# Performance work log

Hardware: AMD Instinct MI355X
Metric: run time of the kernel (lower is better)

The kernel has to match this reference:

```python
import jax, jax.numpy as jnp
import numpy as np

H = 800          # config.param.hidden_size (768 bert + 32 pos)
BERT_H = 768
POS_DIM = 32
NHEAD = 8
DH = 100         # gat_nhidden; NHEAD*DH == H
GAT_LAYERS = 2
N_EVENTS = 66
N_ROLES = 122
EPS = 0.1        # label smoothing
NEG_SLOPE = 0.2  # GATConv leaky_relu slope


def bilstm(x, Wih_f, Whh_f, b_f, Wih_b, Whh_b, b_b):
    """x: [B,T,D] -> [B,T,2H] (torch gate order i,f,g,o)."""
    def run(xs, Wih, Whh, b):
        B = xs.shape[1]; Hd = Whh.shape[1]
        def step(carry, xt):
            h, c = carry
            g = xt @ Wih.T + h @ Whh.T + b
            i, f, gg, o = jnp.split(g, 4, axis=-1)
            c = jax.nn.sigmoid(f) * c + jax.nn.sigmoid(i) * jnp.tanh(gg)
            h = jax.nn.sigmoid(o) * jnp.tanh(c)
            return (h, c), h
        init = (jnp.zeros((B, Hd), xs.dtype), jnp.zeros((B, Hd), xs.dtype))
        _, hs = jax.lax.scan(step, init, xs)
        return hs
    xt = jnp.swapaxes(x, 0, 1)                      # [T,B,D]
    hf = run(xt, Wih_f, Whh_f, b_f)
    hb = run(xt[::-1], Wih_b, Whh_b, b_b)[::-1]
    return jnp.swapaxes(jnp.concatenate([hf, hb], -1), 0, 1)


def gat_conv(x, src, dst, W, a_src, a_dst, bias):
    """PyG GATConv, concat heads, with self-loops. x:[n,H], src/dst:[E]."""
    n = x.shape[0]
    loops = jnp.arange(n)
    s = jnp.concatenate([src, loops])
    d = jnp.concatenate([dst, loops])
    h = (x @ W).reshape(n, NHEAD, DH)
    a_s = jnp.einsum('nhd,hd->nh', h, a_src)
    a_d = jnp.einsum('nhd,hd->nh', h, a_dst)
    e = jax.nn.leaky_relu(a_s[s] + a_d[d], NEG_SLOPE)              # [E,nh]
    m = jnp.full((n, NHEAD), -jnp.inf, x.dtype).at[d].max(e)       # segment max
    ex = jnp.exp(e - m[d])
    den = jnp.zeros((n, NHEAD), x.dtype).at[d].add(ex)
    alpha = ex / den[d]
    out = jnp.zeros((n, NHEAD, DH), x.dtype).at[d].add(alpha[..., None] * h[s])
    return out.reshape(n, NHEAD * DH) + bias


def label_smooth_ce(logits, target):
    c = logits.shape[-1]
    logp = jax.nn.log_softmax(logits, axis=-1)
    smooth = -logp.sum(-1)
    nll = -jnp.take_along_axis(logp, target[..., None], axis=-1)[..., 0]
    return smooth * EPS / c + (1.0 - EPS) * nll


def setup_inputs() -> dict:
    key = jax.random.key(0)
    ks = iter(jax.random.split(key, 32))
    B, S, E = 4, 128, 256
    std = 0.02
    inp = {}
    inp['bert_out'] = jax.random.normal(next(ks), (B, S + 1, BERT_H), jnp.float32)
    inp['pos_ids'] = jax.random.randint(next(ks), (B, S), 0, 31)
    inp['edge_src'] = jax.random.randint(next(ks), (B, E), 0, S)
    inp['edge_dst'] = jax.random.randint(next(ks), (B, E), 0, S)
    inp['start_labels'] = jax.random.randint(next(ks), (B, S, S), 0, N_EVENTS)
    inp['end_labels'] = jax.random.randint(next(ks), (B, S, S), 0, N_EVENTS)
    # parameters
    inp['pos_table'] = std * jax.random.normal(next(ks), (31, POS_DIM), jnp.float32)
    for sfx in ('f', 'b'):
        inp[f'Wih_{sfx}'] = std * jax.random.normal(next(ks), (4 * H, H), jnp.float32)
        inp[f'Whh_{sfx}'] = std * jax.random.normal(next(ks), (4 * H, H), jnp.float32)
        inp[f'bl_{sfx}'] = jnp.zeros((4 * H,), jnp.float32)
    inp['lstm_fc_W'] = std * jax.random.normal(next(ks), (2 * H, H), jnp.float32)
    inp['lstm_fc_b'] = jnp.zeros((H,), jnp.float32)
    inp['table_W'] = std * jax.random.normal(next(ks), (2 * H, H), jnp.float32)
    inp['table_b'] = jnp.zeros((H,), jnp.float32)
    inp['gat_W'] = std * jax.random.normal(next(ks), (H, NHEAD * DH), jnp.float32)
    inp['gat_asrc'] = std * jax.random.normal(next(ks), (NHEAD, DH), jnp.float32)
    inp['gat_adst'] = std * jax.random.normal(next(ks), (NHEAD, DH), jnp.float32)
    inp['gat_bias'] = jnp.zeros((NHEAD * DH,), jnp.float32)
    inp['trig_W'] = std * jax.random.normal(next(ks), (H, N_EVENTS), jnp.float32)
    inp['trig_b'] = jnp.zeros((N_EVENTS,), jnp.float32)
    inp['rs_W'] = std * jax.random.normal(next(ks), (H, N_ROLES), jnp.float32)
    inp['rs_b'] = jnp.zeros((N_ROLES,), jnp.float32)
    inp['re_W'] = std * jax.random.normal(next(ks), (H, N_ROLES), jnp.float32)
    inp['re_b'] = jnp.zeros((N_ROLES,), jnp.float32)
    return inp


def reference(bert_out, pos_ids, edge_src, edge_dst, start_labels, end_labels,
              pos_table, Wih_f, Whh_f, bl_f, Wih_b, Whh_b, bl_b,
              lstm_fc_W, lstm_fc_b, table_W, table_b,
              gat_W, gat_asrc, gat_adst, gat_bias,
              trig_W, trig_b, rs_W, rs_b, re_W, re_b):
    B, S = pos_ids.shape
    # POS embedding, prepend zero vector for [CLS] position
    pos_emb = pos_table[pos_ids]                                   # [B,S,32]
    pos_emb = jnp.concatenate(
        [jnp.zeros((B, 1, POS_DIM), bert_out.dtype), pos_emb], axis=1)
    x = jnp.concatenate([bert_out, pos_emb], axis=-1)              # [B,S+1,800]
    lstm_out = bilstm(x, Wih_f, Whh_f, bl_f, Wih_b, Whh_b, bl_b)   # [B,S+1,1600]
    x = x + jax.nn.relu(lstm_out @ lstm_fc_W + lstm_fc_b)
    x = x[:, 1:, :]                                                # drop CLS -> [B,S,800]

    # per-sample residual GAT stack (eval mode: dropout is identity)
    def gat_stack(xi, si, di):
        for _ in range(GAT_LAYERS):
            xi = xi + jax.nn.relu(gat_conv(xi, si, di, gat_W, gat_asrc, gat_adst, gat_bias))
        return xi
    x = jax.vmap(gat_stack)(x, edge_src, edge_dst)                 # [B,S,800]

    # pairwise table: cat(x_i, x_j) -> fc -> gelu
    x1 = jnp.broadcast_to(x[:, :, None, :], (B, S, S, H))
    x2 = jnp.broadcast_to(x[:, None, :, :], (B, S, S, H))
    s_tab = jax.nn.gelu(jnp.concatenate([x1, x2], -1) @ table_W + table_b)  # [B,S,S,800]

    eye = jnp.eye(S, dtype=start_labels.dtype)
    trig_mask = eye                                                # [S,S]
    arg_mask = 1 - eye
    trig_maskf = trig_mask.astype(s_tab.dtype)
    arg_maskf = arg_mask.astype(s_tab.dtype)

    trig_logits = s_tab @ trig_W + trig_b                          # [B,S,S,66]
    arg1_logits = s_tab @ rs_W + rs_b                              # [B,S,S,122]
    arg2_logits = s_tab @ re_W + re_b

    def masked_mean(loss, maskf):
        return (loss * maskf).sum((1, 2)) / maskf.sum()

    l1 = masked_mean(label_smooth_ce(trig_logits, start_labels * trig_mask), trig_maskf)
    l2 = masked_mean(label_smooth_ce(arg1_logits, start_labels * arg_mask), arg_maskf)
    l3 = masked_mean(label_smooth_ce(arg2_logits, end_labels * arg_mask), arg_maskf)
    total_loss = (l1 + l2 + l3).sum()

    trig_pred = jnp.argmax(trig_logits, -1)
    a1_pred = jnp.argmax(arg1_logits + jnp.swapaxes(arg1_logits, 1, 2), -1)
    a2_pred = jnp.argmax(arg2_logits + jnp.swapaxes(arg2_logits, 1, 2), -1)
    results1 = trig_pred * trig_mask + a1_pred * arg_mask
    results2 = trig_pred * trig_mask + a2_pred * arg_mask
    return total_loss, results1, results2
```

## Files before the change

### kernel.cpp

```cpp
#include <hip/hip_runtime.h>
#include <hip/hip_bf16.h>

#define B4 4
#define S128 128
#define T129 129
#define H800 800
#define E256 256
#define NE 66
#define NR 122
#define DPW 8
#define NWGD 100
#define FSTR 32

typedef float f32x4 __attribute__((ext_vector_type(4)));

#define HB_ROW 900

__device__ __forceinline__ float gelu_f(float x) {
    float t = 0.7978845608028654f * (x + 0.044715f * x * x * x);
    float e = __expf(2.f * t);
    float th = 1.f - 2.f / (e + 1.f);
    return 0.5f * x * (1.f + th);
}

__device__ __forceinline__ float embed_at(const float* __restrict__ bert,
                                          const int* __restrict__ pids,
                                          const float* __restrict__ ptab,
                                          int m, int c)
{
    if (c < 768) return bert[(size_t)m * 768 + c];
    int t = m % T129, b = m / T129;
    if (t == 0) return 0.f;
    return ptab[pids[b * S128 + t - 1] * 32 + (c - 768)];
}

template<int AMODE, int BTRANS, int EPI>
__global__ __launch_bounds__(256) void k_gemm(const float* __restrict__ A, const float* __restrict__ Bm,
                                              const float* __restrict__ bias, const float* __restrict__ res,
                                              float* __restrict__ C, int M, int N, int K)
{
    __shared__ float As[16][68];
    __shared__ float Bs[16][68];
    int m0 = blockIdx.x * 64, n0 = blockIdx.y * 64;
    int tid = threadIdx.x;
    int tm = tid & 15, tn = tid >> 4;
    float acc[4][4] = {};
    for (int k0 = 0; k0 < K; k0 += 16) {
        {
            int kk = tid & 15, mmb = tid >> 4;
            #pragma unroll
            for (int q = 0; q < 4; q++) {
                int mm = mmb + q * 16;
                int m = m0 + mm;
                float v = 0.f;
                if (m < M) {
                    int row = (AMODE == 1) ? (m + (m >> 7) + 1) : m;
                    v = A[(size_t)row * K + k0 + kk];
                }
                As[kk][mm] = v;
            }
        }
        if (BTRANS == 0) {
            int nn = (tid & 15) * 4, kk2 = tid >> 4;
            int n = n0 + nn;
            float t0, t1, t2, t3;
            if (n + 3 < N) {
                const float4 bv = *(const float4*)&Bm[(size_t)(k0 + kk2) * N + n];
                t0 = bv.x; t1 = bv.y; t2 = bv.z; t3 = bv.w;
            } else {
                t0 = (n + 0 < N) ? Bm[(size_t)(k0 + kk2) * N + n + 0] : 0.f;
                t1 = (n + 1 < N) ? Bm[(size_t)(k0 + kk2) * N + n + 1] : 0.f;
                t2 = (n + 2 < N) ? Bm[(size_t)(k0 + kk2) * N + n + 2] : 0.f;
                t3 = (n + 3 < N) ? Bm[(size_t)(k0 + kk2) * N + n + 3] : 0.f;
            }
            Bs[kk2][nn + 0] = t0; Bs[kk2][nn + 1] = t1; Bs[kk2][nn + 2] = t2; Bs[kk2][nn + 3] = t3;
        } else {
            int kk = tid & 15, nnb = tid >> 4;
            #pragma unroll
            for (int q = 0; q < 4; q++) {
                int nn = nnb + q * 16;
                int n = n0 + nn;
                Bs[kk][nn] = (n < N) ? Bm[(size_t)n * K + k0 + kk] : 0.f;
            }
        }
        __syncthreads();
        #pragma unroll
        for (int kk = 0; kk < 16; kk++) {
            float4 a = *(const float4*)&As[kk][tm * 4];
            float4 bb = *(const float4*)&Bs[kk][tn * 4];
            float av[4] = {a.x, a.y, a.z, a.w};
            float bv[4] = {bb.x, bb.y, bb.z, bb.w};
            #pragma unroll
            for (int xx = 0; xx < 4; xx++)
                #pragma unroll
                for (int yy = 0; yy < 4; yy++)
                    acc[xx][yy] += av[xx] * bv[yy];
        }
        __syncthreads();
    }
    #pragma unroll
    for (int xx = 0; xx < 4; xx++) {
        int m = m0 + tm * 4 + xx;
        if (m >= M) continue;
        #pragma unroll
        for (int yy = 0; yy < 4; yy++) {
            int n = n0 + tn * 4 + yy;
            if (n >= N) continue;
            float v = acc[xx][yy];
            if (bias) v += bias[n];
            if (EPI == 1) v = res[(size_t)m * N + n] + fmaxf(v, 0.f);
            C[(size_t)m * N + n] = v;
        }
    }
}

__global__ __launch_bounds__(256) void k_gemm_wih(const float* __restrict__ bert,
                                                  const int* __restrict__ pids,
                                                  const float* __restrict__ ptab,
                                                  const float* __restrict__ Wf, const float* __restrict__ Wb,
                                                  const float* __restrict__ bf, const float* __restrict__ bb_,
                                                  float* __restrict__ C)
{
    __shared__ float As[16][68];
    __shared__ float Bs[16][68];
    const int M = 516, K = 800, N = 6400;
    int m0 = blockIdx.x * 64, n0 = blockIdx.y * 64;
    const float* W  = (n0 < 3200) ? Wf : Wb;
    const float* bi = (n0 < 3200) ? bf : bb_;
    int nb = (n0 < 3200) ? n0 : (n0 - 3200);
    int tid = threadIdx.x;
    int tm = tid & 15, tn = tid >> 4;
    int kk_s = tid & 15, mmb = tid >> 4;
    int mrow[4]; int pofs[4]; bool mok[4];
    #pragma unroll
    for (int q = 0; q < 4; q++) {
        int m = m0 + mmb + q * 16;
        mrow[q] = m;
        mok[q] = m < M;
        int t = m % T129, b = m / T129;
        pofs[q] = (mok[q] && t > 0) ? pids[b * S128 + t - 1] * 32 : -1;
    }
    float acc[4][4] = {};
    for (int k0 = 0; k0 < K; k0 += 16) {
        {
            int c = k0 + kk_s;
            #pragma unroll
            for (int q = 0; q < 4; q++) {
                float v = 0.f;
                if (mok[q]) {
                    if (c < 768) v = bert[(size_t)mrow[q] * 768 + c];
                    else         v = (pofs[q] < 0) ? 0.f : ptab[pofs[q] + c - 768];
                }
                As[kk_s][mmb + q * 16] = v;
            }
        }
        {
            int kk = tid & 15, nnb = tid >> 4;
            #pragma unroll
            for (int q = 0; q < 4; q++) {
                int nn = nnb + q * 16;
                Bs[kk][nn] = W[(size_t)(nb + nn) * K + k0 + kk];
            }
        }
        __syncthreads();
        #pragma unroll
        for (int kk = 0; kk < 16; kk++) {
            float4 a = *(const float4*)&As[kk][tm * 4];
            float4 bb = *(const float4*)&Bs[kk][tn * 4];
            float av[4] = {a.x, a.y, a.z, a.w};
            float bv[4] = {bb.x, bb.y, bb.z, bb.w};
            #pragma unroll
            for (int xx = 0; xx < 4; xx++)
                #pragma unroll
                for (int yy = 0; yy < 4; yy++)
                    acc[xx][yy] += av[xx] * bv[yy];
        }
        __syncthreads();
    }
    #pragma unroll
    for (int xx = 0; xx < 4; xx++) {
        int m = m0 + tm * 4 + xx;
        if (m >= M) continue;
        #pragma unroll
        for (int yy = 0; yy < 4; yy++) {
            int n = n0 + tn * 4 + yy;
            C[(size_t)m * N + n] = acc[xx][yy] + bi[nb + (n - n0)];
        }
    }
}

__global__ __launch_bounds__(256) void k_gemm_fc(const float* __restrict__ A, const float* __restrict__ Bm,
                                                 const float* __restrict__ bias,
                                                 const float* __restrict__ bert, const int* __restrict__ pids,
                                                 const float* __restrict__ ptab, float* __restrict__ C)
{
    __shared__ float As[16][68];
    __shared__ float Bs[16][68];
    const int M = 516, N = 800, K = 1600;
    int m0 = blockIdx.x * 64, n0 = blockIdx.y * 64;
    int tid = threadIdx.x;
    int tm = tid & 15, tn = tid >> 4;
    float acc[4][4] = {};
    for (int k0 = 0; k0 < K; k0 += 16) {
        {
            int kk = tid & 15, mmb = tid >> 4;
            #pragma unroll
            for (int q = 0; q < 4; q++) {
                int mm = mmb + q * 16;
                int m = m0 + mm;
                As[kk][mm] = (m < M) ? A[(size_t)m * K + k0 + kk] : 0.f;
            }
        }
        {
            int nn = (tid & 15) * 4, kk2 = tid >> 4;
            int n = n0 + nn;
            if (n + 3 < N) {
                *(float4*)&Bs[kk2][nn] = *(const float4*)&Bm[(size_t)(k0 + kk2) * N + n];
            } else {
                #pragma unroll
                for (int q = 0; q < 4; q++)
                    Bs[kk2][nn + q] = (n + q < N) ? Bm[(size_t)(k0 + kk2) * N + n + q] : 0.f;
            }
        }
        __syncthreads();
        #pragma unroll
        for (int kk = 0; kk < 16; kk++) {
            float4 a = *(const float4*)&As[kk][tm * 4];
            float4 bb = *(const float4*)&Bs[kk][tn * 4];
            float av[4] = {a.x, a.y, a.z, a.w};
            float bv[4] = {bb.x, bb.y, bb.z, bb.w};
            #pragma unroll
            for (int xx = 0; xx < 4; xx++)
                #pragma unroll
                for (int yy = 0; yy < 4; yy++)
                    acc[xx][yy] += av[xx] * bv[yy];
        }
        __syncthreads();
    }
    #pragma unroll
    for (int xx = 0; xx < 4; xx++) {
        int m = m0 + tm * 4 + xx;
        if (m >= M) continue;
        #pragma unroll
        for (int yy = 0; yy < 4; yy++) {
            int n = n0 + tn * 4 + yy;
            if (n >= N) continue;
            float v = fmaxf(acc[xx][yy] + bias[n], 0.f);
            C[(size_t)m * N + n] = embed_at(bert, pids, ptab, m, n) + v;
        }
    }
}

__global__ __launch_bounds__(256) void k_gemm_uv(const float* __restrict__ A, const float* __restrict__ tW,
                                                 const float* __restrict__ tb, float* __restrict__ C)
{
    __shared__ float As[16][68];
    __shared__ float Bs[16][68];
    const int M = 512, K = 800, N = 1600;
    int m0 = blockIdx.x * 64, n0 = blockIdx.y * 64;
    int tid = threadIdx.x;
    int tm = tid & 15, tn = tid >> 4;
    float acc[4][4] = {};
    for (int k0 = 0; k0 < K; k0 += 16) {
        {
            int kk = tid & 15, mmb = tid >> 4;
            #pragma unroll
            for (int q = 0; q < 4; q++) {
                int mm = mmb + q * 16;
                As[kk][mm] = A[(size_t)(m0 + mm) * K + k0 + kk];
            }
        }
        {
            int nn = (tid & 15) * 4, kk2 = tid >> 4;
            #pragma unroll
            for (int q = 0; q < 4; q++) {
                int n = n0 + nn + q;
                Bs[kk2][nn + q] = (n < 800) ? tW[(size_t)(k0 + kk2) * 800 + n]
                                            : tW[(size_t)(800 + k0 + kk2) * 800 + (n - 800)];
            }
        }
        __syncthreads();
        #pragma unroll
        for (int kk = 0; kk < 16; kk++) {
            float4 a = *(const float4*)&As[kk][tm * 4];
            float4 bb = *(const float4*)&Bs[kk][tn * 4];
            float av[4] = {a.x, a.y, a.z, a.w};
            float bv[4] = {bb.x, bb.y, bb.z, bb.w};
            #pragma unroll
            for (int xx = 0; xx < 4; xx++)
                #pragma unroll
                for (int yy = 0; yy < 4; yy++)
                    acc[xx][yy] += av[xx] * bv[yy];
        }
        __syncthreads();
    }
    #pragma unroll
    for (int xx = 0; xx < 4; xx++) {
        int m = m0 + tm * 4 + xx;
        #pragma unroll
        for (int yy = 0; yy < 4; yy++) {
            int n = n0 + tn * 4 + yy;
            float v = acc[xx][yy];
            if (n < 800) v += tb[n];
            C[(size_t)m * N + n] = v;
        }
    }
}

__global__ __launch_bounds__(256) void k_lstm(const float* __restrict__ xW,
                                              const float* __restrict__ Whhf, const float* __restrict__ Whhb,
                                              float* __restrict__ lstm, float* __restrict__ hpk,
                                              int* __restrict__ flags)
{
    __shared__ float hb[4][HB_ROW];
    __shared__ float gsum[25][32][4];
    __shared__ float gg[128];
    int wg = blockIdx.x;
    int dir = wg >= NWGD ? 1 : 0;
    int wgd = dir ? wg - NWGD : wg;
    const float* Whh = dir ? Whhb : Whhf;
    const float* xWd = xW + dir * 3200;
    int tid = threadIdx.x;
    bool dotth = tid < 200;
    int d = tid & 7, sl = tid >> 3;
    int k0 = sl * 32;
    int rb = tid & 3, rd = (tid >> 2) & 7, rg = tid >> 5;
    int lane = tid & 63;

    float wreg[4][32];
    if (dotth) {
        #pragma unroll
        for (int g = 0; g < 4; g++) {
            const float* wp = Whh + (size_t)(g * 800 + wgd * DPW + d) * 800 + k0;
            #pragma unroll
            for (int q = 0; q < 32; q += 4)
                *(float4*)&wreg[g][q] = *(const float4*)&wp[q];
        }
    }
    for (int i = tid; i < 4 * HB_ROW; i += 256) (&hb[0][0])[i] = 0.f;
    __syncthreads();

    float cst = 0.f;
    int fid = dir * NWGD + wgd;

    for (int step = 0; step < 129; step++) {
        int t = dir ? (128 - step) : step;
        float xq = 0.f;
        if (tid < 128)
            xq = xWd[(size_t)(rb * T129 + t) * 6400 + rg * 800 + wgd * DPW + rd];
        if (step > 0) {
            if (tid < 64) {
                bool mine = (lane < 25);
                int base = dir * NWGD + lane * 4;
                long long iters = 0;
                for (;;) {
                    int mn = step;
                    if (mine) {
                        int f0 = __hip_atomic_load(&flags[(base + 0) * FSTR], __ATOMIC_RELAXED, __HIP_MEMORY_SCOPE_AGENT);
                        int f1 = __hip_atomic_load(&flags[(base + 1) * FSTR], __ATOMIC_RELAXED, __HIP_MEMORY_SCOPE_AGENT);
                        int f2 = __hip_atomic_load(&flags[(base + 2) * FSTR], __ATOMIC_RELAXED, __HIP_MEMORY_SCOPE_AGENT);
                        int f3 = __hip_atomic_load(&flags[(base + 3) * FSTR], __ATOMIC_RELAXED, __HIP_MEMORY_SCOPE_AGENT);
                        mn = min(min(f0, f1), min(f2, f3));
                    }
                    if (__all(mn >= step)) break;
                    if (++iters > 50000000LL) break;
                }
            }
            __syncthreads();
            int tprev = dir ? (t + 1) : (t - 1);
            if (tid < 200) {
                const f32x4* pb = (const f32x4*)(hpk + (size_t)(dir * 129 + tprev) * 3200);
                const f32x4* p0 = pb + tid;
                const f32x4* p1 = pb + tid + 200;
                const f32x4* p2 = pb + tid + 400;
                const f32x4* p3 = pb + tid + 600;
                f32x4 v0, v1, v2, v3;
                asm volatile(
                    "global_load_dwordx4 %0, %4, off sc0 sc1\n\t"
                    "global_load_dwordx4 %1, %5, off sc0 sc1\n\t"
                    "global_load_dwordx4 %2, %6, off sc0 sc1\n\t"
                    "global_load_dwordx4 %3, %7, off sc0 sc1\n\t"
                    "s_waitcnt vmcnt(0)"
                    : "=&v"(v0), "=&v"(v1), "=&v"(v2), "=&v"(v3)
                    : "v"(p0), "v"(p1), "v"(p2), "v"(p3)
                    : "memory");
                {
                    int s0 = tid;
                    int p_ = (s0 >> 3) * 8 + (s0 & 1) * 4;
                    ((f32x4*)&hb[0][0])[((s0 & 7) >> 1) * 225 + (p_ >> 5) * 9 + ((p_ & 31) >> 2)] = v0;
                }
                {
                    int s1 = tid + 200;
                    int p_ = (s1 >> 3) * 8 + (s1 & 1) * 4;
                    ((f32x4*)&hb[0][0])[((s1 & 7) >> 1) * 225 + (p_ >> 5) * 9 + ((p_ & 31) >> 2)] = v1;
                }
                {
                    int s2 = tid + 400;
                    int p_ = (s2 >> 3) * 8 + (s2 & 1) * 4;
                    ((f32x4*)&hb[0][0])[((s2 & 7) >> 1) * 225 + (p_ >> 5) * 9 + ((p_ & 31) >> 2)] = v2;
                }
                {
                    int s3 = tid + 600;
                    int p_ = (s3 >> 3) * 8 + (s3 & 1) * 4;
                    ((f32x4*)&hb[0][0])[((s3 & 7) >> 1) * 225 + (p_ >> 5) * 9 + ((p_ & 31) >> 2)] = v3;
                }
            }
            __syncthreads();
        }
        if (dotth) {
            float a[4][4] = {};
            #pragma unroll
            for (int b = 0; b < 4; b++) {
                const float* hrow = &hb[b][0];
                #pragma unroll
                for (int q = 0; q < 32; q += 4) {
                    float4 h = *(const float4*)&hrow[sl * 36 + q];
                    #pragma unroll
                    for (int g = 0; g < 4; g++)
                        a[g][b] += wreg[g][q] * h.x + wreg[g][q + 1] * h.y
                                 + wreg[g][q + 2] * h.z + wreg[g][q + 3] * h.w;
                }
            }
            #pragma unroll
            for (int g = 0; g < 4; g++)
                *(float4*)&gsum[sl][g * 8 + d][0] = make_float4(a[g][0], a[g][1], a[g][2], a[g][3]);
        }
        __syncthreads();
        if (tid < 128) {
            float s = xq;
            #pragma unroll
            for (int ss = 0; ss < 25; ss++) s += gsum[ss][rg * 8 + rd][rb];
            gg[tid] = s;
        }
        __syncthreads();
        float hv = 0.f;
        if (tid < 32) {
            int dd = tid & 7, bb2 = tid >> 3;
            float gi = gg[(0 << 5) | (dd << 2) | bb2];
            float gf = gg[(1 << 5) | (dd << 2) | bb2];
            float gG = gg[(2 << 5) | (dd << 2) | bb2];
            float go = gg[(3 << 5) | (dd << 2) | bb2];
            float si = 1.f / (1.f + __expf(-gi));
            float sf = 1.f / (1.f + __expf(-gf));
            float so = 1.f / (1.f + __expf(-go));
            cst = sf * cst + si * tanhf(gG);
            hv = so * tanhf(cst);
        }
        if (tid < 64) {
            int src = (lane & 7) * 4;
            f32x4 o;
            o.x = __shfl(hv, src + 0, 64);
            o.y = __shfl(hv, src + 1, 64);
            o.z = __shfl(hv, src + 2, 64);
            o.w = __shfl(hv, src + 3, 64);
            if (lane < 8) {
                float* pp = hpk + ((size_t)(dir * 129 + t) * 100 + wgd) * 32 + lane * 4;
                asm volatile("global_store_dwordx4 %0, %1, off sc0 sc1"
                             :: "v"((f32x4*)pp), "v"(o) : "memory");
            }
            asm volatile("s_waitcnt vmcnt(0)" ::: "memory");
            if (tid == 0 && step < 128)
                __hip_atomic_store(&flags[fid * FSTR], step + 1,
                                   __ATOMIC_RELAXED, __HIP_MEMORY_SCOPE_AGENT);
            if (lane < 8) {
                int bb = lane >> 1, half = lane & 1;
                float* ap = lstm + (size_t)((bb * T129 + t) * 1600) + dir * 800 + wgd * DPW + half * 4;
                asm volatile("global_store_dwordx4 %0, %1, off sc0 sc1"
                             :: "v"((f32x4*)ap), "v"(o) : "memory");
            }
        }
    }
}

template<int RESMODE>
__global__ __launch_bounds__(512) void k_gat_fused(const int* __restrict__ esrc, const int* __restrict__ edst,
                                                   const float* __restrict__ h1,
                                                   const float* __restrict__ asrc, const float* __restrict__ adst,
                                                   const float* __restrict__ gbias,
                                                   const float* __restrict__ res, float* __restrict__ out)
{
    __shared__ int se[384], de[384];
    __shared__ float asl[128], adl[128], ml[128], dl_[128];
    int bh = blockIdx.x;
    int b = bh >> 3, h = bh & 7;
    int t = threadIdx.x;
    if (t < 384) {
        if (t < E256) { se[t] = esrc[b * E256 + t]; de[t] = edst[b * E256 + t]; }
        else          { se[t] = t - E256;           de[t] = t - E256; }
    }
    int node = t >> 2, ch = t & 3;
    int dd0 = ch * 25;
    {
        const float* hp = h1 + (size_t)(b * S128 + node) * H800 + h * 100 + dd0;
        const float* ap = asrc + h * 100 + dd0;
        const float* dp = adst + h * 100 + dd0;
        float s1 = 0.f, s2 = 0.f;
        #pragma unroll
        for (int q = 0; q < 25; q++) { float hv = hp[q]; s1 += hv * ap[q]; s2 += hv * dp[q]; }
        s1 += __shfl_xor(s1, 1, 64); s1 += __shfl_xor(s1, 2, 64);
        s2 += __shfl_xor(s2, 1, 64); s2 += __shfl_xor(s2, 2, 64);
        if (ch == 0) { asl[node] = s1; adl[node] = s2; }
    }
    __syncthreads();
    if (t < 128) {
        float myad = adl[t];
        float m = -3.4e38f;
        for (int e = 0; e < 384; e++)
            if (de[e] == t) {
                float sc = asl[se[e]] + myad;
                sc = (sc > 0.f) ? sc : 0.2f * sc;
                m = fmaxf(m, sc);
            }
        float den = 0.f;
        for (int e = 0; e < 384; e++)
            if (de[e] == t) {
                float sc = asl[se[e]] + myad;
                sc = (sc > 0.f) ? sc : 0.2f * sc;
                den += __expf(sc - m);
            }
        ml[t] = m; dl_[t] = den;
    }
    __syncthreads();
    float acc[25] = {};
    float myad = adl[node], mym = ml[node];
    for (int e = 0; e < 384; e++) {
        if (de[e] == node) {
            int s = se[e];
            float sc = asl[s] + myad;
            sc = (sc > 0.f) ? sc : 0.2f * sc;
            float w = __expf(sc - mym);
            const float* hp = h1 + (size_t)(b * S128 + s) * H800 + h * 100 + dd0;
            #pragma unroll
            for (int q = 0; q < 25; q++) acc[q] += w * hp[q];
        }
    }
    float inv = 1.f / dl_[node];
    int n = b * S128 + node;
    size_t rrow = (RESMODE == 1) ? (size_t)(n + b + 1) * H800 : (size_t)n * H800;
    #pragma unroll
    for (int q = 0; q < 25; q++) {
        int col = h * 100 + dd0 + q;
        float v = acc[q] * inv + gbias[col];
        out[(size_t)n * H800 + col] = res[rrow + col] + fmaxf(v, 0.f);
    }
}

__global__ __launch_bounds__(64) void k_trig(const float* __restrict__ uv,
                                             const float* __restrict__ W, const float* __restrict__ bias,
                                             const int* __restrict__ labels, float* __restrict__ d_out)
{
    __shared__ float s[800];
    __shared__ float lg[66];
    int bi = blockIdx.x;
    int i = bi & 127;
    int l = threadIdx.x;
    const float* ur = uv + (size_t)bi * 1600;
    const float* vr = ur + 800;
    for (int k = l; k < 800; k += 64) s[k] = gelu_f(ur[k] + vr[k]);
    __syncthreads();
    float a0 = 0.f, a1 = 0.f;
    bool has2 = (l < 2);
    for (int k = 0; k < 800; k++) {
        float sv = s[k];
        a0 += sv * W[k * NE + l];
        if (has2) a1 += sv * W[k * NE + 64 + l];
    }
    lg[l] = a0 + bias[l];
    if (has2) lg[64 + l] = a1 + bias[64 + l];
    __syncthreads();
    if (l == 0) {
        float m = lg[0];
        for (int c = 1; c < NE; c++) m = fmaxf(m, lg[c]);
        float se = 0.f, sl = 0.f, bv = lg[0];
        int am = 0;
        for (int c = 0; c < NE; c++) {
            se += __expf(lg[c] - m);
            sl += lg[c];
            if (lg[c] > bv) { bv = lg[c]; am = c; }
        }
        float lse = m + __logf(se);
        int tgt = labels[(size_t)bi * S128 + i];
        float ce = (0.1f / NE) * (NE * lse - sl) + 0.9f * (lse - lg[tgt]);
        atomicAdd(d_out, ce * (1.f / 128.f));
        int r = bi * S128 + i;
        d_out[1 + r] = (float)am;
        d_out[1 + 65536 + r] = (float)am;
    }
}

__global__ __launch_bounds__(256) void k_logits2(const float* __restrict__ uvb,
                                                 const float* __restrict__ rsW, const float* __restrict__ rsb,
                                                 const float* __restrict__ reW, const float* __restrict__ reb,
                                                 float* __restrict__ L)
{
    __shared__ float As[16][68];
    __shared__ float Bs[16][256];
    int bi = blockIdx.y;
    const float* base = uvb + (size_t)bi * 128 * 1600;
    float* Lb = L + (size_t)bi * 16384 * 256;
    int il = blockIdx.x >> 1;
    int j0 = (blockIdx.x & 1) * 64;
    const float* urow = base + (size_t)il * 1600;
    int tid = threadIdx.x;
    int tm = tid & 7, tn = tid >> 3;
    float acc[8][8] = {};
    int ct = tid;
    int hc = (ct < 128) ? ct : (ct - 128);
    const float* Wp = (ct < 128) ? rsW : reW;
    bool cok = hc < NR;
    for (int k0 = 0; k0 < 800; k0 += 16) {
        {
            int kk = tid & 15, rrb = tid >> 4;
            float uk = urow[k0 + kk];
            #pragma unroll
            for (int q = 0; q < 4; q++) {
                int rr = rrb + q * 16;
                float xv = uk + base[(size_t)(j0 + rr) * 1600 + 800 + k0 + kk];
                As[kk][rr] = gelu_f(xv);
            }
        }
        #pragma unroll
        for (int kk2 = 0; kk2 < 16; kk2++)
            Bs[kk2][ct] = cok ? Wp[(size_t)(k0 + kk2) * NR + hc] : 0.f;
        __syncthreads();
        #pragma unroll
        for (int kk = 0; kk < 16; kk++) {
            float4 a0 = *(const float4*)&As[kk][tm * 8];
            float4 a1 = *(const float4*)&As[kk][tm * 8 + 4];
            float4 b0 = *(const float4*)&Bs[kk][tn * 8];
            float4 b1 = *(const float4*)&Bs[kk][tn * 8 + 4];
            float av[8] = {a0.x, a0.y, a0.z, a0.w, a1.x, a1.y, a1.z, a1.w};
            float bv[8] = {b0.x, b0.y, b0.z, b0.w, b1.x, b1.y, b1.z, b1.w};
            #pragma unroll
            for (int xx = 0; xx < 8; xx++)
                #pragma unroll
                for (int yy = 0; yy < 8; yy++)
                    acc[xx][yy] += av[xx] * bv[yy];
        }
        __syncthreads();
    }
    int head = tn >> 4;
    const float* bp = head ? reb : rsb;
    #pragma unroll
    for (int xx = 0; xx < 8; xx++) {
        int r = il * S128 + j0 + tm * 8 + xx;
        float* Lr = Lb + (size_t)r * 256 + tn * 8;
        #pragma unroll
        for (int hf = 0; hf < 2; hf++) {
            int c = (tn * 8 + hf * 4) & 127;
            if (c + 3 < NR) {
                float4 o = make_float4(acc[xx][hf*4+0] + bp[c+0], acc[xx][hf*4+1] + bp[c+1],
                                       acc[xx][hf*4+2] + bp[c+2], acc[xx][hf*4+3] + bp[c+3]);
                *(float4*)(Lr + hf * 4) = o;
            } else {
                #pragma unroll
                for (int q = 0; q < 4; q++)
                    if (c + q < NR) Lr[hf * 4 + q] = acc[xx][hf*4+q] + bp[c+q];
            }
        }
    }
}

__global__ __launch_bounds__(256) void k_loss2(const float* __restrict__ L,
                                               const int* __restrict__ lab0, const int* __restrict__ lab1,
                                               float* __restrict__ res0, float* __restrict__ res1,
                                               float* __restrict__ lossptr)
{
    __shared__ float wsum[4];
    int wv = threadIdx.x >> 6, l = threadIdx.x & 63;
    int rr = blockIdx.x * 4 + wv;
    int bi = rr >> 14;
    int r = rr & 16383;
    int i = r >> 7, j = r & 127;
    size_t bioff = (size_t)bi * 16384;
    float ces = 0.f;
    if (i != j) {
        const float* row  = L + (bioff + r) * 256;
        const float* prow = L + (bioff + ((j << 7) | i)) * 256;
        bool v2 = (l < NR - 64);
        #pragma unroll
        for (int hd = 0; hd < 2; hd++) {
            const float* rw = row + hd * 128;
            const float* pw = prow + hd * 128;
            float x1 = rw[l];
            float x2 = v2 ? rw[l + 64] : -3.4e38f;
            float m = fmaxf(x1, x2);
            #pragma unroll
            for (int s = 32; s; s >>= 1) m = fmaxf(m, __shfl_xor(m, s, 64));
            float se = __expf(x1 - m) + (v2 ? __expf(x2 - m) : 0.f);
            float sl = x1 + (v2 ? x2 : 0.f);
            #pragma unroll
            for (int s = 32; s; s >>= 1) { se += __shfl_xor(se, s, 64); sl += __shfl_xor(sl, s, 64); }
            float lse = m + __logf(se);
            int tgt = (hd ? lab1 : lab0)[bioff + r];
            float lt = rw[tgt];
            ces += (0.1f / NR) * (NR * lse - sl) + 0.9f * (lse - lt);
            float y1 = x1 + pw[l];
            float y2 = v2 ? (x2 + pw[l + 64]) : -3.4e38f;
            float bv; int bidx;
            if (y2 > y1) { bv = y2; bidx = l + 64; } else { bv = y1; bidx = l; }
            #pragma unroll
            for (int s = 32; s; s >>= 1) {
                float ov = __shfl_xor(bv, s, 64);
                int oi = __shfl_xor(bidx, s, 64);
                if (ov > bv || (ov == bv && oi < bidx)) { bv = ov; bidx = oi; }
            }
            if (l == 0) (hd ? res1 : res0)[bioff + r] = (float)bidx;
        }
    }
    if (l == 0) wsum[wv] = ces;
    __syncthreads();
    if (threadIdx.x == 0) {
        float s = (wsum[0] + wsum[1] + wsum[2] + wsum[3]) * (1.f / 16256.f);
        atomicAdd(lossptr, s);
    }
}

extern "C" void kernel_launch(void* const* d_in, const int* in_sizes, int n_in,
                              void* d_out, int out_size, void* d_ws, size_t ws_size,
                              hipStream_t stream)
{
    (void)in_sizes; (void)n_in; (void)out_size; (void)ws_size;
    const float* bert  = (const float*)d_in[0];
    const int*   pids  = (const int*)d_in[1];
    const int*   esrc  = (const int*)d_in[2];
    const int*   edst  = (const int*)d_in[3];
    const int*   slab  = (const int*)d_in[4];
    const int*   elab  = (const int*)d_in[5];
    const float* ptab  = (const float*)d_in[6];
    const float* Wih_f = (const float*)d_in[7];
    const float* Whh_f = (const float*)d_in[8];
    const float* bl_f  = (const float*)d_in[9];
    const float* Wih_b = (const float*)d_in[10];
    const float* Whh_b = (const float*)d_in[11];
    const float* bl_b  = (const float*)d_in[12];
    const float* fcW   = (const float*)d_in[13];
    const float* fcb   = (const float*)d_in[14];
    const float* tW    = (const float*)d_in[15];
    const float* tb    = (const float*)d_in[16];
    const float* gatW  = (const float*)d_in[17];
    const float* asrc  = (const float*)d_in[18];
    const float* adst  = (const float*)d_in[19];
    const float* gbias = (const float*)d_in[20];
    const float* trigW = (const float*)d_in[21];
    const float* trigb = (const float*)d_in[22];
    const float* rsW   = (const float*)d_in[23];
    const float* rsb   = (const float*)d_in[24];
    const float* reW   = (const float*)d_in[25];
    const float* reb   = (const float*)d_in[26];
    float* out = (float*)d_out;

    float* ws = (float*)d_ws;
    size_t off = 0;
    auto alloc = [&](size_t n) { float* p = ws + off; off += (n + 255) & ~(size_t)255; return p; };
    float* uv    = alloc((size_t)512 * 1600);
    int*   flags = (int*)alloc(2 * NWGD * FSTR);
    float* R     = ws + off;
    size_t roff = 0;
    auto ralloc = [&](size_t n) { float* p = R + roff; roff += (n + 255) & ~(size_t)255; return p; };
    float* xW   = ralloc((size_t)516 * 6400);
    float* lstm = ralloc((size_t)516 * 1600);
    float* xg   = ralloc(516 * 800);
    float* h1   = ralloc(512 * 800);
    float* g1   = ralloc(512 * 800);
    float* g2   = ralloc(512 * 800);
    float* hpk  = ralloc((size_t)2 * 129 * 100 * 32);
    float* Lbuf = R;

    hipMemsetAsync(d_out, 0, 4, stream);
    hipMemsetAsync(flags, 0, 2 * NWGD * FSTR * sizeof(int), stream);

    k_gemm_wih<<<dim3(9, 100), 256, 0, stream>>>(bert, pids, ptab, Wih_f, Wih_b, bl_f, bl_b, xW);

    k_lstm<<<2 * NWGD, 256, 0, stream>>>(xW, Whh_f, Whh_b, lstm, hpk, flags);

    k_gemm_fc<<<dim3(9, 13), 256, 0, stream>>>(lstm, fcW, fcb, bert, pids, ptab, xg);

    k_gemm<1, 0, 0><<<dim3(8, 13), 256, 0, stream>>>(xg, gatW, nullptr, nullptr, h1, 512, 800, 800);
    k_gat_fused<1><<<32, 512, 0, stream>>>(esrc, edst, h1, asrc, adst, gbias, xg, g1);
    k_gemm<0, 0, 0><<<dim3(8, 13), 256, 0, stream>>>(g1, gatW, nullptr, nullptr, h1, 512, 800, 800);
    k_gat_fused<0><<<32, 512, 0, stream>>>(esrc, edst, h1, asrc, adst, gbias, g1, g2);

    k_gemm_uv<<<dim3(8, 25), 256, 0, stream>>>(g2, tW, tb, uv);

    k_trig<<<512, 64, 0, stream>>>(uv, trigW, trigb, slab, out);

    for (int bp = 0; bp < 2; bp++) {
        k_logits2<<<dim3(256, 2), 256, 0, stream>>>(uv + (size_t)bp * 2 * 128 * 1600,
                                                    rsW, rsb, reW, reb, Lbuf);
        k_loss2<<<8192, 256, 0, stream>>>(Lbuf,
                                          slab + (size_t)bp * 2 * 16384, elab + (size_t)bp * 2 * 16384,
                                          out + 1 + (size_t)bp * 2 * 16384,
                                          out + 1 + 65536 + (size_t)bp * 2 * 16384, out);
    }
}
```

Baseline: 2.240 ms.

## Replace per-step flag polling with sentinel-valued hidden-state polling in LSTM

Drops the per-workgroup step flags and their atomic store/poll handshake in the persistent LSTM kernel. The hidden-state exchange buffer is now prefilled with a large sentinel (0x7F bytes), and each consumer spins on the hidden-state loads until every value is below 1.5 in magnitude, which is valid because LSTM outputs lie in (-1,1). This removes one round-trip, the store-wait and the barrier per timestep, at the cost of an extra memset of the buffer and reliance on the sentinel check and on stores becoming visible as whole vectors.

Measured after the change: 2.190 ms. 1.02x faster.

```diff
diff --git a/kernel.cpp b/kernel.cpp
--- a/kernel.cpp
+++ b/kernel.cpp
@@ -10,7 +10,6 @@
 #define NR 122
 #define DPW 8
 #define NWGD 100
-#define FSTR 32
 
 typedef float f32x4 __attribute__((ext_vector_type(4)));
 
@@ -309,8 +308,7 @@
 
 __global__ __launch_bounds__(256) void k_lstm(const float* __restrict__ xW,
                                               const float* __restrict__ Whhf, const float* __restrict__ Whhb,
-                                              float* __restrict__ lstm, float* __restrict__ hpk,
-                                              int* __restrict__ flags)
+                                              float* __restrict__ lstm, float* __restrict__ hpk)
 {
     __shared__ float hb[4][HB_ROW];
     __shared__ float gsum[25][32][4];
@@ -341,7 +339,6 @@
     __syncthreads();
 
     float cst = 0.f;
-    int fid = dir * NWGD + wgd;
 
     for (int step = 0; step < 129; step++) {
         int t = dir ? (128 - step) : step;
@@ -349,24 +346,6 @@
         if (tid < 128)
             xq = xWd[(size_t)(rb * T129 + t) * 6400 + rg * 800 + wgd * DPW + rd];
         if (step > 0) {
-            if (tid < 64) {
-                bool mine = (lane < 25);
-                int base = dir * NWGD + lane * 4;
-                long long iters = 0;
-                for (;;) {
-                    int mn = step;
-                    if (mine) {
-                        int f0 = __hip_atomic_load(&flags[(base + 0) * FSTR], __ATOMIC_RELAXED, __HIP_MEMORY_SCOPE_AGENT);
-                        int f1 = __hip_atomic_load(&flags[(base + 1) * FSTR], __ATOMIC_RELAXED, __HIP_MEMORY_SCOPE_AGENT);
-                        int f2 = __hip_atomic_load(&flags[(base + 2) * FSTR], __ATOMIC_RELAXED, __HIP_MEMORY_SCOPE_AGENT);
-                        int f3 = __hip_atomic_load(&flags[(base + 3) * FSTR], __ATOMIC_RELAXED, __HIP_MEMORY_SCOPE_AGENT);
-                        mn = min(min(f0, f1), min(f2, f3));
-                    }
-                    if (__all(mn >= step)) break;
-                    if (++iters > 50000000LL) break;
-                }
-            }
-            __syncthreads();
             int tprev = dir ? (t + 1) : (t - 1);
             if (tid < 200) {
                 const f32x4* pb = (const f32x4*)(hpk + (size_t)(dir * 129 + tprev) * 3200);
@@ -375,15 +354,28 @@
                 const f32x4* p2 = pb + tid + 400;
                 const f32x4* p3 = pb + tid + 600;
                 f32x4 v0, v1, v2, v3;
-                asm volatile(
-                    "global_load_dwordx4 %0, %4, off sc0 sc1\n\t"
-                    "global_load_dwordx4 %1, %5, off sc0 sc1\n\t"
-                    "global_load_dwordx4 %2, %6, off sc0 sc1\n\t"
-                    "global_load_dwordx4 %3, %7, off sc0 sc1\n\t"
-                    "s_waitcnt vmcnt(0)"
-                    : "=&v"(v0), "=&v"(v1), "=&v"(v2), "=&v"(v3)
-                    : "v"(p0), "v"(p1), "v"(p2), "v"(p3)
-                    : "memory");
+                long long iters = 0;
+                for (;;) {
+                    asm volatile(
+                        "global_load_dwordx4 %0, %4, off sc0 sc1\n\t"
+                        "global_load_dwordx4 %1, %5, off sc0 sc1\n\t"
+                        "global_load_dwordx4 %2, %6, off sc0 sc1\n\t"
+                        "global_load_dwordx4 %3, %7, off sc0 sc1\n\t"
+                        "s_waitcnt vmcnt(0)"
+                        : "=&v"(v0), "=&v"(v1), "=&v"(v2), "=&v"(v3)
+                        : "v"(p0), "v"(p1), "v"(p2), "v"(p3)
+                        : "memory");
+                    bool ok = fabsf(v0.x) < 1.5f && fabsf(v0.y) < 1.5f &&
+                              fabsf(v0.z) < 1.5f && fabsf(v0.w) < 1.5f &&
+                              fabsf(v1.x) < 1.5f && fabsf(v1.y) < 1.5f &&
+                              fabsf(v1.z) < 1.5f && fabsf(v1.w) < 1.5f &&
+                              fabsf(v2.x) < 1.5f && fabsf(v2.y) < 1.5f &&
+                              fabsf(v2.z) < 1.5f && fabsf(v2.w) < 1.5f &&
+                              fabsf(v3.x) < 1.5f && fabsf(v3.y) < 1.5f &&
+                              fabsf(v3.z) < 1.5f && fabsf(v3.w) < 1.5f;
+                    if (ok) break;
+                    if (++iters > 20000000LL) break;
+                }
                 {
                     int s0 = tid;
                     int p_ = (s0 >> 3) * 8 + (s0 & 1) * 4;
@@ -458,10 +450,6 @@
                 asm volatile("global_store_dwordx4 %0, %1, off sc0 sc1"
                              :: "v"((f32x4*)pp), "v"(o) : "memory");
             }
-            asm volatile("s_waitcnt vmcnt(0)" ::: "memory");
-            if (tid == 0 && step < 128)
-                __hip_atomic_store(&flags[fid * FSTR], step + 1,
-                                   __ATOMIC_RELAXED, __HIP_MEMORY_SCOPE_AGENT);
             if (lane < 8) {
                 int bb = lane >> 1, half = lane & 1;
                 float* ap = lstm + (size_t)((bb * T129 + t) * 1600) + dir * 800 + wgd * DPW + half * 4;
@@ -754,7 +742,6 @@
     size_t off = 0;
     auto alloc = [&](size_t n) { float* p = ws + off; off += (n + 255) & ~(size_t)255; return p; };
     float* uv    = alloc((size_t)512 * 1600);
-    int*   flags = (int*)alloc(2 * NWGD * FSTR);
     float* R     = ws + off;
     size_t roff = 0;
     auto ralloc = [&](size_t n) { float* p = R + roff; roff += (n + 255) & ~(size_t)255; return p; };
@@ -768,11 +755,11 @@
     float* Lbuf = R;
 
     hipMemsetAsync(d_out, 0, 4, stream);
-    hipMemsetAsync(flags, 0, 2 * NWGD * FSTR * sizeof(int), stream);
+    hipMemsetAsync(hpk, 0x7F, (size_t)2 * 129 * 100 * 32 * sizeof(float), stream);
 
     k_gemm_wih<<<dim3(9, 100), 256, 0, stream>>>(bert, pids, ptab, Wih_f, Wih_b, bl_f, bl_b, xW);
 
-    k_lstm<<<2 * NWGD, 256, 0, stream>>>(xW, Whh_f, Whh_b, lstm, hpk, flags);
+    k_lstm<<<2 * NWGD, 256, 0, stream>>>(xW, Whh_f, Whh_b, lstm, hpk);
 
     k_gemm_fc<<<dim3(9, 13), 256, 0, stream>>>(lstm, fcW, fcb, bert, pids, ptab, xg);
 
```
